# Optimization experiments

Measured on AMD Instinct MI355X. Metric: run time of the kernel, lower is better.

## Reference

```python
import jax, jax.numpy as jnp
import numpy as np

B, N, C, H = 8, 1025, 1024, 16
DH = C // H
HID = 4 * C
EPS = 1e-5
NEG = -65504.0


def _ln(x, g, b):
    mu = jnp.mean(x, axis=-1, keepdims=True)
    var = jnp.mean(jnp.square(x - mu), axis=-1, keepdims=True)
    return (x - mu) * jax.lax.rsqrt(var + EPS) * g + b


def setup_inputs() -> dict:
    key = jax.random.key(0)
    ks = jax.random.split(key, 12)
    s = 0.02
    return {
        "x": jax.random.normal(ks[0], (B, N, C), jnp.float32),
        "rel_pos_bias": jax.random.normal(ks[1], (H, N, N), jnp.float32),
        "attn_mask": jnp.zeros((B, N, N), jnp.bool_),
        "ln1_g": jnp.ones((C,), jnp.float32),
        "ln1_b": jnp.zeros((C,), jnp.float32),
        "qkv_w": jax.random.normal(ks[2], (C, 3 * C), jnp.float32) * s,
        "qkv_b": jnp.zeros((3 * C,), jnp.float32),
        "proj_w": jax.random.normal(ks[3], (C, C), jnp.float32) * s,
        "proj_b": jnp.zeros((C,), jnp.float32),
        "ln2_g": jnp.ones((C,), jnp.float32),
        "ln2_b": jnp.zeros((C,), jnp.float32),
        "fc1_w": jax.random.normal(ks[4], (C, HID), jnp.float32) * s,
        "fc1_b": jnp.zeros((HID,), jnp.float32),
        "fc2_w": jax.random.normal(ks[5], (HID, C), jnp.float32) * s,
        "fc2_b": jnp.zeros((C,), jnp.float32),
    }


def reference(x, rel_pos_bias, attn_mask, ln1_g, ln1_b, qkv_w, qkv_b,
              proj_w, proj_b, ln2_g, ln2_b, fc1_w, fc1_b, fc2_w, fc2_b):
    scale = DH ** -0.5
    # --- attention branch ---
    h = _ln(x, ln1_g, ln1_b)
    qkv = (h @ qkv_w + qkv_b).reshape(B, N, 3, H, DH)
    q, k, v = [jnp.transpose(qkv[:, :, i], (0, 2, 1, 3)) for i in range(3)]  # [B,H,N,DH]
    attn = jnp.einsum('bhnd,bhmd->bhnm', q * scale, k)
    attn = jnp.where(attn_mask[:, None], NEG, attn)
    attn = attn + rel_pos_bias  # [H,N,N] broadcasts over batch
    attn_wo_softmax = attn
    a = jax.nn.softmax(attn, axis=-1)
    o = jnp.einsum('bhnm,bhmd->bhnd', a, v)
    o = jnp.transpose(o, (0, 2, 1, 3)).reshape(B, N, C)
    o = o @ proj_w + proj_b
    x = x + o
    # --- MLP branch ---
    h2 = _ln(x, ln2_g, ln2_b)
    h2 = jax.nn.gelu(h2 @ fc1_w + fc1_b, approximate=False)
    x = x + (h2 @ fc2_w + fc2_b)
    return (x, attn_wo_softmax)
```

## Files before the change

kernel.cpp:

```cpp
#include <hip/hip_runtime.h>
#include <math.h>

typedef unsigned short u16;
typedef unsigned char u8;
typedef unsigned int u32;
typedef __attribute__((ext_vector_type(4))) float f32x4;
typedef __attribute__((ext_vector_type(4), aligned(4))) float f32x4u;
typedef __attribute__((ext_vector_type(8))) short s16x8;

#define DEV __device__ __forceinline__

constexpr int BB = 8, NN = 1025, CC = 1024, HH = 16;
constexpr int NP  = 1152;
constexpr int MP  = 8320;
constexpr int TOK = BB * NN;
constexpr int MW  = 36;
constexpr float NEGV = -65504.f;

DEV u16 f2bf(float f){ union { float f; unsigned u; } v; v.f = f; return (u16)((v.u + 0x7fffu + ((v.u >> 16) & 1u)) >> 16); }
DEV float bf2f(u16 u){ union { float f; unsigned u; } v; v.u = (unsigned)u << 16; return v.f; }
DEV u32 cvt_pk_bf16(float lo_, float hi_){
  u32 r; asm("v_cvt_pk_bf16_f32 %0, %1, %2" : "=v"(r) : "v"(lo_), "v"(hi_)); return r;
}

struct __align__(8) us4 { u16 x, y, z, w; };

typedef const __attribute__((address_space(1))) void gv_t;
typedef __attribute__((address_space(3))) void lv_t;
DEV void gload16(const void* g, void* l){
  __builtin_amdgcn_global_load_lds((gv_t*)g, (lv_t*)l, 16, 0, 0);
}

__launch_bounds__(256)
__global__ void cvt_transpose(const float* __restrict__ W, u16* __restrict__ Wt, int K, int Nn){
  __shared__ float tile[32][33];
  const int n0 = blockIdx.x * 32, k0 = blockIdx.y * 32;
  const int tx = threadIdx.x & 31, ty = threadIdx.x >> 5;
#pragma unroll
  for (int i = 0; i < 4; i++)
    tile[ty + i * 8][tx] = W[(size_t)(k0 + ty + i * 8) * Nn + n0 + tx];
  __syncthreads();
#pragma unroll
  for (int i = 0; i < 4; i++){
    const int n = n0 + ty + i * 8;
    Wt[(size_t)n * K + k0 + tx] = f2bf(tile[tx][ty + i * 8]);
  }
}

__launch_bounds__(256)
__global__ void ln_kernel(const float* __restrict__ x, const float* __restrict__ g,
                          const float* __restrict__ b, u16* __restrict__ out, int validRows){
  const int row = blockIdx.x, tid = threadIdx.x;
  const size_t base = (size_t)row * CC + tid * 4;
  if (row >= validRows){ us4 z{0,0,0,0}; *(us4*)(out + base) = z; return; }
  f32x4u v = *(const f32x4u*)(x + base);
  float s  = v[0] + v[1] + v[2] + v[3];
  float ss = v[0]*v[0] + v[1]*v[1] + v[2]*v[2] + v[3]*v[3];
#pragma unroll
  for (int o = 32; o; o >>= 1){ s += __shfl_xor(s, o, 64); ss += __shfl_xor(ss, o, 64); }
  __shared__ float ps[4], pq[4];
  if ((tid & 63) == 0){ ps[tid >> 6] = s; pq[tid >> 6] = ss; }
  __syncthreads();
  s  = ps[0] + ps[1] + ps[2] + ps[3];
  ss = pq[0] + pq[1] + pq[2] + pq[3];
  const float mu = s * (1.f / CC);
  const float rs = rsqrtf(ss * (1.f / CC) - mu * mu + 1e-5f);
  f32x4u gv = *(const f32x4u*)(g + tid * 4);
  f32x4u bv = *(const f32x4u*)(b + tid * 4);
  us4 o;
  o.x = f2bf((v[0]-mu)*rs*gv[0] + bv[0]);
  o.y = f2bf((v[1]-mu)*rs*gv[1] + bv[1]);
  o.z = f2bf((v[2]-mu)*rs*gv[2] + bv[2]);
  o.w = f2bf((v[3]-mu)*rs*gv[3] + bv[3]);
  *(us4*)(out + base) = o;
}

template<int MODE>
__launch_bounds__(256)
__global__ void gemm_nt(const u16* __restrict__ A, const u16* __restrict__ Bt,
                        const float* __restrict__ bias, int K, int Nw,
                        const float* __restrict__ resid, float* __restrict__ fout,
                        u16* __restrict__ bout){
  __shared__ u16 As[128 * 32];
  __shared__ u16 Bs[128 * 32];
  const int tid = threadIdx.x;
  const int w = tid >> 6, l = tid & 63;
  const int wr = w >> 1, wc = w & 1;
  const int row0 = blockIdx.y * 128, col0 = blockIdx.x * 128;
  f32x4 acc[4][4] = {};
  for (int k0 = 0; k0 < K; k0 += 32){
    __syncthreads();
#pragma unroll
    for (int j = 0; j < 2; j++){
      const int ch = tid + j * 256;
      const int r = ch >> 2, co = (ch & 3) * 8;
      gload16(A  + (size_t)(row0 + r) * K + k0 + co, As + (size_t)ch * 8);
      gload16(Bt + (size_t)(col0 + r) * K + k0 + co, Bs + (size_t)ch * 8);
    }
    __syncthreads();
    s16x8 af[4], bf[4];
#pragma unroll
    for (int m = 0; m < 4; m++)
      af[m] = *(const s16x8*)(As + (wr * 64 + m * 16 + (l & 15)) * 32 + (l >> 4) * 8);
#pragma unroll
    for (int n = 0; n < 4; n++)
      bf[n] = *(const s16x8*)(Bs + (wc * 64 + n * 16 + (l & 15)) * 32 + (l >> 4) * 8);
#pragma unroll
    for (int m = 0; m < 4; m++)
#pragma unroll
      for (int n = 0; n < 4; n++)
        acc[m][n] = __builtin_amdgcn_mfma_f32_16x16x32_bf16(af[m], bf[n], acc[m][n], 0, 0, 0);
  }
#pragma unroll
  for (int m = 0; m < 4; m++){
#pragma unroll
    for (int n = 0; n < 4; n++){
      const int c = col0 + wc * 64 + n * 16 + (l & 15);
      const float bs = bias[c];
#pragma unroll
      for (int j = 0; j < 4; j++){
        const int r = row0 + wr * 64 + m * 16 + ((l >> 4) << 2) + j;
        float v = acc[m][n][j] + bs;
        if (MODE == 0){
          bout[(size_t)r * Nw + c] = f2bf(v);
        } else if (MODE == 1){
          const float xi = (r < TOK) ? resid[(size_t)r * CC + c] : 0.f;
          fout[(size_t)r * CC + c] = xi + v;
        } else if (MODE == 2){
          const float gx = 0.5f * v * (1.f + erff(v * 0.70710678118654752f));
          bout[(size_t)r * Nw + c] = f2bf(gx);
        } else {
          if (r < TOK) fout[(size_t)r * CC + c] = resid[(size_t)r * CC + c] + v;
        }
      }
    }
  }
}

__launch_bounds__(256)
__global__ void reorder_qkv(const u16* __restrict__ qkv, u16* __restrict__ q,
                            u16* __restrict__ k, u16* __restrict__ vT){
  __shared__ u16 vt[64][65];
  const int bh = blockIdx.y, b = bh >> 4, h = bh & 15;
  const int n0 = blockIdx.x * 64;
  const int tid = threadIdx.x;
  const int d = tid & 63, nl = tid >> 6;
#pragma unroll
  for (int i = 0; i < 16; i++){
    const int nlocal = nl * 16 + i;
    const int n = n0 + nlocal;
    u16 qv = 0, kv = 0, vv = 0;
    if (n < NN){
      const size_t t = (size_t)b * NN + n;
      const u16* p = qkv + t * 3072 + h * 64 + d;
      qv = f2bf(bf2f(p[0]) * 0.125f);
      kv = p[1024];
      vv = p[2048];
    }
    q[(size_t)bh * NP * 64 + (size_t)n * 64 + d] = qv;
    k[(size_t)bh * NP * 64 + (size_t)n * 64 + d] = kv;
    vt[nlocal][d] = vv;
  }
  __syncthreads();
#pragma unroll
  for (int i = 0; i < 16; i++){
    const int dd = (tid >> 6) * 16 + i;
    const int nn2 = tid & 63;
    vT[(size_t)bh * 64 * NP + (size_t)dd * NP + n0 + nn2] = vt[nn2][dd];
  }
}

__launch_bounds__(256)
__global__ void mask_pack(const u8* __restrict__ mask, u32* __restrict__ mbits){
  const int idx = blockIdx.x * 256 + threadIdx.x;
  if (idx >= BB * NP * MW) return;
  const int word = idx % MW;
  const int row  = (idx / MW) % NP;
  const int b    = idx / (MW * NP);
  u32 bits = 0;
  if (row < NN){
    const u8* mrow = mask + (size_t)b * NN * NN + (size_t)row * NN;
    const int c0 = word * 32;
    const int lim = (NN - c0 < 32) ? (NN - c0) : 32;
    for (int j = 0; j < lim; j++) bits |= (u32)(mrow[c0 + j] != 0) << j;
  }
  mbits[idx] = bits;
}

__launch_bounds__(256)
__global__ void attn_flash(const u16* __restrict__ q, const u16* __restrict__ k,
                           const u16* __restrict__ vT, const float* __restrict__ bias,
                           const u32* __restrict__ mbits,
                           float* __restrict__ S, u16* __restrict__ obuf){
  __shared__ u16 Ks[128 * 64];
  __shared__ u16 Vs[64 * 128];

  const int f = blockIdx.x;
  const int xcd = f & 7, ii = f >> 3;
  const int hl = ii / 144, rem = ii % 144;
  const int rt = rem >> 3, b = rem & 7;
  const int h = xcd * 2 + hl;
  const int bh = b * 16 + h;
  const int tid = threadIdx.x, w = tid >> 6, l = tid & 63;
  const int lg = l >> 4, lo = l & 15;
  const int row0 = rt * 64 + w * 16;
  const u16* qb = q + (size_t)bh * NP * 64;
  const u16* kb = k + (size_t)bh * NP * 64;
  const u16* vb = vT + (size_t)bh * 64 * NP;
  const float* bias_h = bias + (size_t)h * NN * NN;
  const u32* mrow_b = mbits + (size_t)b * NP * MW;
  float* Sb = S + (size_t)bh * NN * NN;

  s16x8 qf[2];
#pragma unroll
  for (int kk = 0; kk < 2; kk++)
    qf[kk] = *(const s16x8*)(qb + (size_t)(row0 + lo) * 64 + kk * 32 + lg * 8);

  float m_run = -1e30f, l_run = 0.f;
  f32x4 acc_o[4] = {};

  for (int ct = 0; ct < 9; ct++){
    const int cb = ct * 128;
    __syncthreads();
#pragma unroll
    for (int i = 0; i < 4; i++){
      const int chunk = tid + i * 256;
      const int row = chunk >> 3, cs = chunk & 7;
      const int cg = cs ^ (row & 7);
      gload16(kb + (size_t)(cb + row) * 64 + cg * 8, Ks + (size_t)chunk * 8);
    }
#pragma unroll
    for (int i = 0; i < 4; i++){
      const int chunk = tid + i * 256;
      const int row = chunk >> 4, cs = chunk & 15;
      const int cg = cs ^ (row & 15);
      gload16(vb + (size_t)row * NP + cb + cg * 8, Vs + (size_t)chunk * 8);
    }
    __syncthreads();

    f32x4 sa[8] = {};
#pragma unroll
    for (int m2 = 0; m2 < 8; m2++){
      const int rl = (m2 >> 1) * 32 + (lo >> 2) * 8 + (m2 & 1) * 4 + (lo & 3);
      const s16x8 kf0 = *(const s16x8*)(Ks + rl * 64 + ((lg ^ (rl & 7)) << 3));
      const s16x8 kf1 = *(const s16x8*)(Ks + rl * 64 + (((4 + lg) ^ (rl & 7)) << 3));
      sa[m2] = __builtin_amdgcn_mfma_f32_16x16x32_bf16(kf0, qf[0], sa[m2], 0, 0, 0);
      sa[m2] = __builtin_amdgcn_mfma_f32_16x16x32_bf16(kf1, qf[1], sa[m2], 0, 0, 0);
    }
    {
      const int qr = row0 + lo;
      if (qr < NN){
        const u32* mrp = mrow_b + (size_t)qr * MW + ct * 4;
        u32 mb[4];
#pragma unroll
        for (int i = 0; i < 4; i++) mb[i] = mrp[i];
        const float* brow = bias_h + (size_t)qr * NN;
        float* srow = Sb + (size_t)qr * NN;
#pragma unroll
        for (int m2 = 0; m2 < 8; m2++){
          const int kc0 = cb + (m2 >> 1) * 32 + lg * 8 + (m2 & 1) * 4;
          const u32 bits = mb[m2 >> 1] >> (lg * 8 + (m2 & 1) * 4);
          f32x4 a = sa[m2];
          if (kc0 + 3 < NN){
            f32x4u bv = *(const f32x4u*)(brow + kc0);
#pragma unroll
            for (int jj = 0; jj < 4; jj++){
              float v = ((bits >> jj) & 1u) ? NEGV : a[jj];
              a[jj] = v + bv[jj];
            }
            *(f32x4u*)(srow + kc0) = a;
          } else {
#pragma unroll
            for (int jj = 0; jj < 4; jj++){
              if (kc0 + jj < NN){
                float v = ((bits >> jj) & 1u) ? NEGV : a[jj];
                v += brow[kc0 + jj];
                srow[kc0 + jj] = v;
                a[jj] = v;
              } else a[jj] = -1e30f;
            }
          }
          sa[m2] = a;
        }
      } else {
        const f32x4 z = {0.f, 0.f, 0.f, 0.f};
#pragma unroll
        for (int m2 = 0; m2 < 8; m2++) sa[m2] = z;
      }
    }
    float sc;
    {
      float mt = -1e30f;
#pragma unroll
      for (int m2 = 0; m2 < 8; m2++){
        f32x4 a = sa[m2];
        mt = fmaxf(mt, fmaxf(fmaxf(a[0], a[1]), fmaxf(a[2], a[3])));
      }
      mt = fmaxf(mt, __shfl_xor(mt, 16, 64));
      mt = fmaxf(mt, __shfl_xor(mt, 32, 64));
      const float mn = fmaxf(m_run, mt);
      sc = __expf(m_run - mn);
      float p = 0.f;
#pragma unroll
      for (int m2 = 0; m2 < 8; m2++){
        f32x4 a = sa[m2];
        const float e0 = __expf(a[0] - mn), e1 = __expf(a[1] - mn);
        const float e2 = __expf(a[2] - mn), e3 = __expf(a[3] - mn);
        p += (e0 + e1) + (e2 + e3);
        sa[m2][0] = __uint_as_float(cvt_pk_bf16(e0, e1));
        sa[m2][1] = __uint_as_float(cvt_pk_bf16(e2, e3));
      }
      p += __shfl_xor(p, 16, 64);
      p += __shfl_xor(p, 32, 64);
      l_run = l_run * sc + p;
      m_run = mn;
    }
#pragma unroll
    for (int jj = 0; jj < 4; jj++){
      const float s = __shfl(sc, (l & 48) + lg * 4 + jj, 64);
#pragma unroll
      for (int nd = 0; nd < 4; nd++) acc_o[nd][jj] *= s;
    }
#pragma unroll
    for (int kc = 0; kc < 4; kc++){
      union { u32 d[4]; s16x8 v8; } af;
      af.d[0] = __float_as_uint(sa[2 * kc][0]);
      af.d[1] = __float_as_uint(sa[2 * kc][1]);
      af.d[2] = __float_as_uint(sa[2 * kc + 1][0]);
      af.d[3] = __float_as_uint(sa[2 * kc + 1][1]);
#pragma unroll
      for (int nd = 0; nd < 4; nd++){
        const int vrow = nd * 16 + lo;
        const s16x8 vf = *(const s16x8*)(Vs + vrow * 128 + (((kc * 4 + lg) ^ (vrow & 15)) << 3));
        acc_o[nd] = __builtin_amdgcn_mfma_f32_16x16x32_bf16(af.v8, vf, acc_o[nd], 0, 0, 0);
      }
    }
  }
  {
    const float li = 1.f / l_run;
#pragma unroll
    for (int jj = 0; jj < 4; jj++){
      const float il = __shfl(li, (l & 48) + lg * 4 + jj, 64);
      const int qr = row0 + lg * 4 + jj;
      if (qr < NN){
        const size_t base = ((size_t)b * NN + qr) * CC + (size_t)h * 64;
#pragma unroll
        for (int nd = 0; nd < 4; nd++)
          obuf[base + nd * 16 + lo] = f2bf(acc_o[nd][jj] * il);
      }
    }
  }
}

__launch_bounds__(256)
__global__ void zero_pad_rows(u16* __restrict__ buf){
  const size_t i = (size_t)blockIdx.x * 256 + threadIdx.x;
  buf[(size_t)TOK * CC + i] = 0;
}

extern "C" void kernel_launch(void* const* d_in, const int* in_sizes, int n_in,
                              void* d_out, int out_size, void* d_ws, size_t ws_size,
                              hipStream_t stream){
  const float* x     = (const float*)d_in[0];
  const float* rpb   = (const float*)d_in[1];
  const u8*    mask  = (const u8*)d_in[2];
  const float* ln1g  = (const float*)d_in[3];
  const float* ln1b  = (const float*)d_in[4];
  const float* qkvw  = (const float*)d_in[5];
  const float* qkvb  = (const float*)d_in[6];
  const float* projw = (const float*)d_in[7];
  const float* projb = (const float*)d_in[8];
  const float* ln2g  = (const float*)d_in[9];
  const float* ln2b  = (const float*)d_in[10];
  const float* fc1w  = (const float*)d_in[11];
  const float* fc1b  = (const float*)d_in[12];
  const float* fc2w  = (const float*)d_in[13];
  const float* fc2b  = (const float*)d_in[14];

  float* out_x = (float*)d_out;
  float* out_S = out_x + (size_t)BB * NN * CC;

  char* wsb = (char*)d_ws;
  size_t off = 0;
  auto alloc = [&](size_t bytes) -> char* {
    char* p = wsb + off; off += (bytes + 255) & ~(size_t)255; return p;
  };
  u16* h1     = (u16*)alloc((size_t)MP * CC * 2);
  u16* qkvbuf = (u16*)alloc((size_t)MP * 3072 * 2);
  u16* h3     = h1;
  u16* qkvwt  = (u16*)alloc((size_t)3072 * 1024 * 2);
  u16* projwt = (u16*)alloc((size_t)1024 * 1024 * 2);
  u16* fc1wt  = (u16*)alloc((size_t)4096 * 1024 * 2);
  u16* fc2wt  = (u16*)alloc((size_t)1024 * 4096 * 2);
  u16* qq     = (u16*)alloc((size_t)128 * NP * 64 * 2);
  u16* kk     = (u16*)alloc((size_t)128 * NP * 64 * 2);
  u16* vT     = (u16*)alloc((size_t)128 * 64 * NP * 2);
  u32* mbits  = (u32*)alloc((size_t)BB * NP * MW * 4);
  u16* obuf   = (u16*)alloc((size_t)MP * CC * 2);
  float* x1   = (float*)alloc((size_t)MP * CC * 4);
  u16* h2in   = (u16*)alloc((size_t)MP * CC * 2);

  cvt_transpose<<<dim3(3072/32, 1024/32), 256, 0, stream>>>(qkvw, qkvwt, 1024, 3072);
  cvt_transpose<<<dim3(1024/32, 1024/32), 256, 0, stream>>>(projw, projwt, 1024, 1024);
  cvt_transpose<<<dim3(4096/32, 1024/32), 256, 0, stream>>>(fc1w, fc1wt, 1024, 4096);
  cvt_transpose<<<dim3(1024/32, 4096/32), 256, 0, stream>>>(fc2w, fc2wt, 4096, 1024);
  ln_kernel<<<MP, 256, 0, stream>>>(x, ln1g, ln1b, h1, TOK);
  gemm_nt<0><<<dim3(3072/128, MP/128), 256, 0, stream>>>(h1, qkvwt, qkvb, 1024, 3072, nullptr, nullptr, qkvbuf);
  reorder_qkv<<<dim3(NP/64, 128), 256, 0, stream>>>(qkvbuf, qq, kk, vT);
  mask_pack<<<(BB * NP * MW + 255) / 256, 256, 0, stream>>>(mask, mbits);
  zero_pad_rows<<<(MP - TOK) * CC / 256, 256, 0, stream>>>(obuf);
  attn_flash<<<dim3(2304), 256, 0, stream>>>(qq, kk, vT, rpb, mbits, out_S, obuf);
  gemm_nt<1><<<dim3(1024/128, MP/128), 256, 0, stream>>>(obuf, projwt, projb, 1024, 1024, x, x1, nullptr);
  ln_kernel<<<MP, 256, 0, stream>>>(x1, ln2g, ln2b, h2in, TOK);
  gemm_nt<2><<<dim3(4096/128, MP/128), 256, 0, stream>>>(h2in, fc1wt, fc1b, 1024, 4096, nullptr, nullptr, h3);
  gemm_nt<3><<<dim3(1024/128, MP/128), 256, 0, stream>>>(h3, fc2wt, fc2b, 4096, 1024, x1, out_x, nullptr);
}
```

Baseline: 888.2 us.

## Transpose score fragments via shuffles for row-coalesced bias loads and score stores

For the first eight key tiles in the attention kernel, each lane's MFMA score fragments are redistributed with cross-lane shuffles so that each group of 8 lanes covers 32 consecutive columns of one query row. The bias read and the attn_wo_softmax write then become row-contiguous 16-byte accesses, and the values are shuffled back into MFMA layout for the softmax. The last, partial tile keeps a simplified scalar path with per-element bounds checks. The aim is to cut scattered global traffic on the large fp32 score output and bias input, at the cost of many extra shuffle instructions and more register pressure.

```diff
diff --git a/kernel.cpp b/kernel.cpp
--- a/kernel.cpp
+++ b/kernel.cpp
@@ -219,6 +219,13 @@
   float m_run = -1e30f, l_run = 0.f;
   f32x4 acc_o[4] = {};
 
+  const int qrow8 = l >> 3;
+  const int c4 = (l & 7) * 4;
+  const int srcF = qrow8 + (((l & 7) >> 1) << 4);
+  const int bsel = (l & 7) & 1;
+  const int lR = (lo & 7) * 8 + (lg << 1);
+  const int hiRow = lo >> 3;
+
   for (int ct = 0; ct < 9; ct++){
     const int cb = ct * 128;
     __syncthreads();
@@ -247,7 +254,52 @@
       sa[m2] = __builtin_amdgcn_mfma_f32_16x16x32_bf16(kf0, qf[0], sa[m2], 0, 0, 0);
       sa[m2] = __builtin_amdgcn_mfma_f32_16x16x32_bf16(kf1, qf[1], sa[m2], 0, 0, 0);
     }
-    {
+
+    if (ct < 8){
+#pragma unroll
+      for (int p = 0; p < 4; p++){
+        f32x4 vA, vB;
+#pragma unroll
+        for (int jj = 0; jj < 4; jj++){
+          const float a0 = __shfl(sa[2*p][jj],     srcF,     64);
+          const float a1 = __shfl(sa[2*p + 1][jj], srcF,     64);
+          const float b0 = __shfl(sa[2*p][jj],     srcF + 8, 64);
+          const float b1 = __shfl(sa[2*p + 1][jj], srcF + 8, 64);
+          vA[jj] = bsel ? a1 : a0;
+          vB[jj] = bsel ? b1 : b0;
+        }
+        const int raA = row0 + qrow8;
+        const int raB = row0 + 8 + qrow8;
+        const int colg = cb + p * 32 + c4;
+        if (raA < NN){
+          const f32x4u bv = *(const f32x4u*)(bias_h + (size_t)raA * NN + colg);
+          const u32 wd = mrow_b[(size_t)raA * MW + ct * 4 + p];
+#pragma unroll
+          for (int jj = 0; jj < 4; jj++)
+            vA[jj] = (((wd >> (c4 + jj)) & 1u) ? NEGV : vA[jj]) + bv[jj];
+          *(f32x4u*)(Sb + (size_t)raA * NN + colg) = vA;
+        } else { vA[0] = vA[1] = vA[2] = vA[3] = -1e30f; }
+        if (raB < NN){
+          const f32x4u bv = *(const f32x4u*)(bias_h + (size_t)raB * NN + colg);
+          const u32 wd = mrow_b[(size_t)raB * MW + ct * 4 + p];
+#pragma unroll
+          for (int jj = 0; jj < 4; jj++)
+            vB[jj] = (((wd >> (c4 + jj)) & 1u) ? NEGV : vB[jj]) + bv[jj];
+          *(f32x4u*)(Sb + (size_t)raB * NN + colg) = vB;
+        } else { vB[0] = vB[1] = vB[2] = vB[3] = -1e30f; }
+#pragma unroll
+        for (int b2 = 0; b2 < 2; b2++){
+          f32x4 outv;
+#pragma unroll
+          for (int jj = 0; jj < 4; jj++){
+            const float fa = __shfl(vA[jj], lR + b2, 64);
+            const float fb = __shfl(vB[jj], lR + b2, 64);
+            outv[jj] = hiRow ? fb : fa;
+          }
+          sa[2*p + b2] = outv;
+        }
+      }
+    } else {
       const int qr = row0 + lo;
       if (qr < NN){
         const u32* mrp = mrow_b + (size_t)qr * MW + ct * 4;
@@ -261,24 +313,14 @@
           const int kc0 = cb + (m2 >> 1) * 32 + lg * 8 + (m2 & 1) * 4;
           const u32 bits = mb[m2 >> 1] >> (lg * 8 + (m2 & 1) * 4);
           f32x4 a = sa[m2];
-          if (kc0 + 3 < NN){
-            f32x4u bv = *(const f32x4u*)(brow + kc0);
-#pragma unroll
-            for (int jj = 0; jj < 4; jj++){
+#pragma unroll
+          for (int jj = 0; jj < 4; jj++){
+            if (kc0 + jj < NN){
               float v = ((bits >> jj) & 1u) ? NEGV : a[jj];
-              a[jj] = v + bv[jj];
-            }
-            *(f32x4u*)(srow + kc0) = a;
-          } else {
-#pragma unroll
-            for (int jj = 0; jj < 4; jj++){
-              if (kc0 + jj < NN){
-                float v = ((bits >> jj) & 1u) ? NEGV : a[jj];
-                v += brow[kc0 + jj];
-                srow[kc0 + jj] = v;
-                a[jj] = v;
-              } else a[jj] = -1e30f;
-            }
+              v += brow[kc0 + jj];
+              srow[kc0 + jj] = v;
+              a[jj] = v;
+            } else a[jj] = -1e30f;
           }
           sa[m2] = a;
         }
@@ -288,6 +330,7 @@
         for (int m2 = 0; m2 < 8; m2++) sa[m2] = z;
       }
     }
+
     float sc;
     {
       float mt = -1e30f;
```

Result: slower. 921.0 us (+3.7%).
